# Kernel optimization log

Measured on AMD Instinct MI355X. Metric: run time of the kernel, lower is better.

Reference implementation:

```python
import jax, jax.numpy as jnp
import numpy as np

B, S, D, V, OOV = 32, 1024, 512, 50000, 1000
BN_EPS = 1e-5


def setup_inputs() -> dict:
    key = jax.random.key(0)
    ks = jax.random.split(key, 24)
    std = 0.02
    inp = {
        'dec_output': jax.random.normal(ks[0], (B, 1, D), jnp.float32),
        'dec_hid_h': jax.random.normal(ks[1], (1, B, D), jnp.float32),
        'dec_hid_c': jax.random.normal(ks[2], (1, B, D), jnp.float32),
        'dec_inp': jax.random.normal(ks[3], (B, 1, D), jnp.float32),
        'enc_op': jax.random.normal(ks[4], (B, S, 2 * D), jnp.float32),
        'enc_op1': jax.random.normal(ks[5], (B, S, 2 * D), jnp.float32),
        'src_inp': jax.random.randint(ks[6], (B, S), 0, V, jnp.int64) if jax.config.jax_enable_x64 else jax.random.randint(ks[6], (B, S), 0, V, jnp.int32),
        # mod_dec_op: Linear(2D -> 2D) with bias
        'W_dec': jax.random.normal(ks[7], (2 * D, 2 * D), jnp.float32) * std,
        'b_dec': jax.random.normal(ks[8], (2 * D,), jnp.float32) * std,
        # get_attn: Linear(2D -> 1), no bias
        'w_attn': jax.random.normal(ks[9], (2 * D,), jnp.float32) * std,
        # get_vocab: Linear(3D -> D) then Linear(D -> V-OOV)
        'W_v1': jax.random.normal(ks[10], (D, 3 * D), jnp.float32) * std,
        'b_v1': jax.random.normal(ks[11], (D,), jnp.float32) * std,
        'W_v2': jax.random.normal(ks[12], (V - OOV, D), jnp.float32) * std,
        'b_v2': jax.random.normal(ks[13], (V - OOV,), jnp.float32) * std,
        # p_gen: sigmoid(Linear([context(2D); dec_state(2D); dec_inp(D)] -> 1))
        'W_p': jax.random.normal(ks[14], (1, 5 * D), jnp.float32) * std,
        'b_p': jax.random.normal(ks[15], (1,), jnp.float32) * std,
        # BatchNorm1d(2D), eval mode
        'bn_gamma': jnp.ones((2 * D,), jnp.float32),
        'bn_beta': jnp.zeros((2 * D,), jnp.float32),
        'bn_mean': jax.random.normal(ks[16], (2 * D,), jnp.float32) * 0.1,
        'bn_var': jax.random.uniform(ks[17], (2 * D,), jnp.float32, 0.5, 1.5),
    }
    return inp


def reference(dec_output, dec_hid_h, dec_hid_c, dec_inp, enc_op, enc_op1, src_inp,
              W_dec, b_dec, w_attn, W_v1, b_v1, W_v2, b_v2, W_p, b_p,
              bn_gamma, bn_beta, bn_mean, bn_var):
    # dec_op: [B, 2D] = [h_b ; c_b]
    dec_op = jnp.concatenate([dec_hid_h[0], dec_hid_c[0]], axis=-1)
    dec_op1 = dec_op @ W_dec.T + b_dec                              # [B, 2D]
    features = jnp.tanh(enc_op1 + dec_op1[:, None, :])              # [B, S, 2D]
    attn = jax.nn.softmax(jnp.einsum('bsd,d->bs', features, w_attn), axis=-1)
    mask = (src_inp != 0).astype(attn.dtype)
    attn = attn * mask
    attn = attn / jnp.sum(attn, axis=1, keepdims=True)              # renormalize
    context = jnp.einsum('bs,bsd->bd', attn, enc_op)                # [B, 2D]
    context = (context - bn_mean) * jax.lax.rsqrt(bn_var + BN_EPS) * bn_gamma + bn_beta
    temp = jnp.concatenate([dec_output[:, 0, :], context], axis=-1)  # [B, 3D]
    logits = (temp @ W_v1.T + b_v1) @ W_v2.T + b_v2                 # [B, V-OOV]
    p_vocab = jax.nn.softmax(logits, axis=-1)
    p_vocab = jnp.concatenate([p_vocab, jnp.zeros((p_vocab.shape[0], OOV), p_vocab.dtype)], axis=-1)
    pg_in = jnp.concatenate([context, dec_op, dec_inp[:, 0, :]], axis=-1)  # [B, 5D]
    p_gen = jax.nn.sigmoid(pg_in @ W_p.T + b_p)                     # [B, 1]
    src_attn = (1.0 - p_gen) * attn                                  # [B, S]
    p_final = p_gen * p_vocab                                        # [B, V]
    rows = jnp.arange(p_final.shape[0])[:, None]
    p_final = p_final.at[rows, src_inp].add(src_attn)
    p_final = p_final + (p_final == 0).astype(p_final.dtype) * 1e-12
    return (p_final, attn, context)
```

## Files before the change

kernel.cpp:

```cpp
#include <hip/hip_runtime.h>

#define B    32
#define S    1024
#define D    512
#define D2   1024
#define D5   2560
#define V    50000
#define VO   49000
#define NCH  14
#define CHW  3500
#define NCHV 766

__device__ __forceinline__ float fast_tanh(float x){
    float e = __expf(2.0f * x);
    return 1.0f - __fdividef(2.0f, e + 1.0f);
}

__global__ __launch_bounds__(256) void gemm_nt(
    const float* __restrict__ W, int Nreal, int K,
    const float* __restrict__ xa, const float* __restrict__ xb,
    int xsplit, int xstra, int xstrb,
    float* __restrict__ parts, int KS)
{
    __shared__ float sW[16 * 260];
    __shared__ float sX[16 * 32];
    const int t    = threadIdx.x;
    const int lane = t & 63;
    const int v0   = blockIdx.x * 256;
    const int ks0  = blockIdx.y * KS;
    const int b0   = (t >> 6) * 8;

    const int vrow  = v0 + t;
    const size_t wb = (size_t)((vrow < Nreal) ? vrow : (Nreal - 1)) * K;

    float acc[4][8];
    #pragma unroll
    for (int i = 0; i < 4; ++i)
        #pragma unroll
        for (int j = 0; j < 8; ++j) acc[i][j] = 0.f;

    const int  xbi  = t >> 2;
    const int  xq   = t & 3;
    const bool xact = t < 128;

    float4 wreg[4];
    float  xreg[4];
    #pragma unroll
    for (int e = 0; e < 4; ++e) wreg[e] = *(const float4*)&W[wb + ks0 + e * 4];
    if (xact){
        #pragma unroll
        for (int e = 0; e < 4; ++e){
            int k = ks0 + xq * 4 + e;
            xreg[e] = (k < xsplit) ? xa[xbi * xstra + k] : xb[xbi * xstrb + (k - xsplit)];
        }
    }

    const int ntiles = KS >> 4;
    for (int tl = 0; tl < ntiles; ++tl){
        #pragma unroll
        for (int e = 0; e < 4; ++e){
            sW[(e * 4 + 0) * 260 + t] = wreg[e].x;
            sW[(e * 4 + 1) * 260 + t] = wreg[e].y;
            sW[(e * 4 + 2) * 260 + t] = wreg[e].z;
            sW[(e * 4 + 3) * 260 + t] = wreg[e].w;
        }
        if (xact){
            #pragma unroll
            for (int e = 0; e < 4; ++e) sX[(xq * 4 + e) * 32 + xbi] = xreg[e];
        }
        __syncthreads();
        if (tl + 1 < ntiles){
            int kn = ks0 + (tl + 1) * 16;
            #pragma unroll
            for (int e = 0; e < 4; ++e) wreg[e] = *(const float4*)&W[wb + kn + e * 4];
            if (xact){
                #pragma unroll
                for (int e = 0; e < 4; ++e){
                    int k = kn + xq * 4 + e;
                    xreg[e] = (k < xsplit) ? xa[xbi * xstra + k] : xb[xbi * xstrb + (k - xsplit)];
                }
            }
        }
        #pragma unroll
        for (int kk = 0; kk < 16; ++kk){
            const float4 w0 = *(const float4*)&sW[kk * 260 + lane * 4];
            const float4 x0 = *(const float4*)&sX[kk * 32 + b0];
            const float4 x1 = *(const float4*)&sX[kk * 32 + b0 + 4];
            const float wv[4] = {w0.x, w0.y, w0.z, w0.w};
            const float xv[8] = {x0.x, x0.y, x0.z, x0.w, x1.x, x1.y, x1.z, x1.w};
            #pragma unroll
            for (int i = 0; i < 4; ++i)
                #pragma unroll
                for (int j = 0; j < 8; ++j)
                    acc[i][j] += wv[i] * xv[j];
        }
        __syncthreads();
    }
    const int vbase = v0 + lane * 4;
    if (vbase < Nreal){
        const size_t pb = (size_t)blockIdx.y * B;
        #pragma unroll
        for (int j = 0; j < 8; ++j){
            float4 o = make_float4(acc[0][j], acc[1][j], acc[2][j], acc[3][j]);
            *(float4*)&parts[(pb + b0 + j) * (size_t)Nreal + vbase] = o;
        }
    }
}

__global__ void kreduce(const float* __restrict__ parts, float* __restrict__ out,
                        int n, int nsplit, const float* __restrict__ bias, int bmask){
    int i = blockIdx.x * 256 + threadIdx.x;
    if (i < n){
        float s = 0.f;
        for (int p = 0; p < nsplit; ++p) s += parts[(size_t)p * n + i];
        if (bias) s += bias[i & bmask];
        out[i] = s;
    }
}

__global__ void k2a_logit(const float* __restrict__ enc1, const float* __restrict__ dop1,
                          const float* __restrict__ bdec, const float* __restrict__ wat,
                          const int* __restrict__ src,
                          float* __restrict__ lg, float* __restrict__ pm,
                          float* __restrict__ ps){
    int b = blockIdx.x;
    int wave = threadIdx.x >> 6, lane = threadIdx.x & 63;
    int s0 = blockIdx.y * 16 + wave * 4;
    __shared__ float sd[D2], sw[D2];
    __shared__ float slog[16];
    for (int i = threadIdx.x; i < D2; i += 256){
        sd[i] = dop1[b * D2 + i] + bdec[i];
        sw[i] = wat[i];
    }
    __syncthreads();
    const float4* sd4 = (const float4*)sd;
    const float4* sw4 = (const float4*)sw;
    for (int r = 0; r < 4; ++r){
        int s = s0 + r;
        const float4* row = (const float4*)(enc1 + ((size_t)b * S + s) * D2);
        float acc = 0.f;
        #pragma unroll
        for (int i = 0; i < 4; ++i){
            int k4 = i * 64 + lane;
            float4 e = row[k4]; float4 dv = sd4[k4]; float4 wv = sw4[k4];
            acc += fast_tanh(e.x + dv.x) * wv.x + fast_tanh(e.y + dv.y) * wv.y
                 + fast_tanh(e.z + dv.z) * wv.z + fast_tanh(e.w + dv.w) * wv.w;
        }
        #pragma unroll
        for (int off = 32; off > 0; off >>= 1) acc += __shfl_down(acc, off, 64);
        if (lane == 0){
            lg[b * S + s] = acc;
            slog[wave * 4 + r] = acc;
        }
    }
    __syncthreads();
    if (threadIdx.x == 0){
        int sbase = blockIdx.y * 16;
        float m = -1e30f;
        #pragma unroll
        for (int i = 0; i < 16; ++i) m = fmaxf(m, slog[i]);
        float sum = 0.f;
        #pragma unroll
        for (int i = 0; i < 16; ++i){
            bool keep = src[b * S + sbase + i] != 0;
            sum += keep ? __expf(slog[i] - m) : 0.f;
        }
        pm[b * 64 + blockIdx.y] = m;
        ps[b * 64 + blockIdx.y] = sum;
    }
}

__global__ void k2c_attn_ctx(const float* __restrict__ enc, const float* __restrict__ lg,
                             const int* __restrict__ src, const float* __restrict__ pm,
                             const float* __restrict__ ps,
                             float* __restrict__ attn, float* __restrict__ part){
    int b = blockIdx.x, sp = blockIdx.y, t = threadIdx.x;
    __shared__ float sa[32];
    __shared__ float sMS[2];
    if (t < 64){
        float m = pm[b * 64 + t];
        float s = ps[b * 64 + t];
        float M = m;
        #pragma unroll
        for (int off = 1; off < 64; off <<= 1) M = fmaxf(M, __shfl_xor(M, off, 64));
        float sv = s * __expf(m - M);
        #pragma unroll
        for (int off = 1; off < 64; off <<= 1) sv += __shfl_xor(sv, off, 64);
        if (t == 0){ sMS[0] = M; sMS[1] = sv; }
    }
    __syncthreads();
    float M   = sMS[0];
    float inv = 1.0f / sMS[1];
    if (t < 32){
        int s = sp * 32 + t;
        float l = lg[b * S + s];
        bool keep = src[b * S + s] != 0;
        float a = keep ? __expf(l - M) * inv : 0.f;
        attn[b * S + s] = a;
        sa[t] = a;
    }
    __syncthreads();
    const float4* base = (const float4*)(enc + ((size_t)b * S + sp * 32) * D2);
    float4 acc = make_float4(0.f, 0.f, 0.f, 0.f);
    #pragma unroll 4
    for (int s = 0; s < 32; ++s){
        float a = sa[s];
        float4 e = base[s * (D2 / 4) + t];
        acc.x += a * e.x; acc.y += a * e.y; acc.z += a * e.z; acc.w += a * e.w;
    }
    ((float4*)(part + ((size_t)(b * 32 + sp)) * D2))[t] = acc;
}

__global__ void k2d_ctxbn(const float* __restrict__ part, const float* __restrict__ gamma,
                          const float* __restrict__ beta, const float* __restrict__ mean,
                          const float* __restrict__ var, float* __restrict__ ctx){
    int b = blockIdx.x, t = threadIdx.x;
    float4 acc = make_float4(0.f, 0.f, 0.f, 0.f);
    for (int sp = 0; sp < 32; ++sp){
        float4 p = ((const float4*)(part + ((size_t)(b * 32 + sp)) * D2))[t];
        acc.x += p.x; acc.y += p.y; acc.z += p.z; acc.w += p.w;
    }
    float4 g  = ((const float4*)gamma)[t];
    float4 be = ((const float4*)beta)[t];
    float4 mn = ((const float4*)mean)[t];
    float4 vr = ((const float4*)var)[t];
    acc.x = (acc.x - mn.x) * rsqrtf(vr.x + 1e-5f) * g.x + be.x;
    acc.y = (acc.y - mn.y) * rsqrtf(vr.y + 1e-5f) * g.y + be.y;
    acc.z = (acc.z - mn.z) * rsqrtf(vr.z + 1e-5f) * g.z + be.z;
    acc.w = (acc.w - mn.w) * rsqrtf(vr.w + 1e-5f) * g.w + be.w;
    ((float4*)(ctx + (size_t)b * D2))[t] = acc;
}

__global__ void k3r_pgen(const float* __restrict__ parts, float* __restrict__ out,
                         const float* __restrict__ bias,
                         const float* __restrict__ ctx, const float* __restrict__ h,
                         const float* __restrict__ c, const float* __restrict__ di,
                         const float* __restrict__ Wp, const float* __restrict__ bp,
                         float* __restrict__ pg){
    int t = threadIdx.x;
    if (blockIdx.x < 64){
        int i = blockIdx.x * 256 + t;
        float s = 0.f;
        for (int p = 0; p < 16; ++p) s += parts[(size_t)p * (B * D) + i];
        s += bias[i & (D - 1)];
        out[i] = s;
        return;
    }
    int b = blockIdx.x - 64;
    float acc = 0.f;
    for (int k = t; k < D5; k += 256){
        float x;
        if (k < D2)            x = ctx[b * D2 + k];
        else if (k < D2 + D)   x = h[b * D + (k - D2)];
        else if (k < 2 * D2)   x = c[b * D + (k - D2 - D)];
        else                   x = di[b * D + (k - 2 * D2)];
        acc += x * Wp[k];
    }
    __shared__ float red[256];
    red[t] = acc; __syncthreads();
    for (int o = 128; o > 0; o >>= 1){
        if (t < o) red[t] += red[t + o];
        __syncthreads();
    }
    if (t == 0){
        float z = red[0] + bp[0];
        pg[b] = 1.0f / (1.0f + __expf(-z));
    }
}

__global__ __launch_bounds__(128) void gemm_vocab64(
    const float* __restrict__ W, const float* __restrict__ hid,
    const float* __restrict__ b2, float* __restrict__ lred,
    float* __restrict__ mch, float* __restrict__ sch)
{
    __shared__ float sW[16 * 68];
    __shared__ float sX[16 * 32];
    const int t    = threadIdx.x;
    const int lane = t & 63;
    const int wave = t >> 6;
    const int v0   = blockIdx.x * 64;

    const int sr   = t & 63;
    const int sh   = (t >> 6) * 8;
    const int vrow = v0 + sr;
    const size_t wb = (size_t)((vrow < VO) ? vrow : (VO - 1)) * D + sh;

    const int xbi = t >> 2;
    const int xq  = (t & 3) * 4;

    float acc[16];
    #pragma unroll
    for (int j = 0; j < 16; ++j) acc[j] = 0.f;

    float4 wreg[2];
    float  xreg[4];
    wreg[0] = *(const float4*)&W[wb];
    wreg[1] = *(const float4*)&W[wb + 4];
    #pragma unroll
    for (int e = 0; e < 4; ++e) xreg[e] = hid[xbi * D + xq + e];

    for (int tl = 0; tl < 32; ++tl){
        sW[(sh + 0) * 68 + sr] = wreg[0].x;
        sW[(sh + 1) * 68 + sr] = wreg[0].y;
        sW[(sh + 2) * 68 + sr] = wreg[0].z;
        sW[(sh + 3) * 68 + sr] = wreg[0].w;
        sW[(sh + 4) * 68 + sr] = wreg[1].x;
        sW[(sh + 5) * 68 + sr] = wreg[1].y;
        sW[(sh + 6) * 68 + sr] = wreg[1].z;
        sW[(sh + 7) * 68 + sr] = wreg[1].w;
        #pragma unroll
        for (int e = 0; e < 4; ++e) sX[(xq + e) * 32 + xbi] = xreg[e];
        __syncthreads();
        if (tl + 1 < 32){
            const int kn = (tl + 1) * 16;
            wreg[0] = *(const float4*)&W[wb + kn];
            wreg[1] = *(const float4*)&W[wb + kn + 4];
            #pragma unroll
            for (int e = 0; e < 4; ++e) xreg[e] = hid[xbi * D + kn + xq + e];
        }
        #pragma unroll
        for (int kk = 0; kk < 16; ++kk){
            const float  w  = sW[kk * 68 + lane];
            const float4 x0 = *(const float4*)&sX[kk * 32 + wave * 16 + 0];
            const float4 x1 = *(const float4*)&sX[kk * 32 + wave * 16 + 4];
            const float4 x2 = *(const float4*)&sX[kk * 32 + wave * 16 + 8];
            const float4 x3 = *(const float4*)&sX[kk * 32 + wave * 16 + 12];
            acc[0]  += w * x0.x; acc[1]  += w * x0.y; acc[2]  += w * x0.z; acc[3]  += w * x0.w;
            acc[4]  += w * x1.x; acc[5]  += w * x1.y; acc[6]  += w * x1.z; acc[7]  += w * x1.w;
            acc[8]  += w * x2.x; acc[9]  += w * x2.y; acc[10] += w * x2.z; acc[11] += w * x2.w;
            acc[12] += w * x3.x; acc[13] += w * x3.y; acc[14] += w * x3.z; acc[15] += w * x3.w;
        }
        __syncthreads();
    }

    const int  va    = v0 + lane;
    const bool valid = va < VO;
    const float b2v  = valid ? b2[va] : 0.f;

    #pragma unroll
    for (int j = 0; j < 16; ++j){
        const int b = wave * 16 + j;
        float l = acc[j] + b2v;
        if (valid) lred[(size_t)b * VO + va] = l;
        float m = valid ? l : -1e30f;
        #pragma unroll
        for (int off = 1; off < 64; off <<= 1) m = fmaxf(m, __shfl_xor(m, off, 64));
        float sv = valid ? __expf(l - m) : 0.f;
        #pragma unroll
        for (int off = 1; off < 64; off <<= 1) sv += __shfl_xor(sv, off, 64);
        if (lane == 0){
            mch[b * NCHV + blockIdx.x] = m;
            sch[b * NCHV + blockIdx.x] = sv;
        }
    }
}

__global__ void kC_final2(const float* __restrict__ lred, const float* __restrict__ mch,
                          const float* __restrict__ sch, const float* __restrict__ pg,
                          float* __restrict__ pf){
    int b = blockIdx.x, c = blockIdx.y, t = threadIdx.x;
    if (c == NCH){
        for (int v = VO + t; v < V; v += 256) pf[(size_t)b * V + v] = 0.f;
        return;
    }
    __shared__ float sm[256], ss[256];
    float m = -1e30f, s = 0.f;
    for (int ch = t; ch < NCHV; ch += 256){
        float mc = mch[b * NCHV + ch], sc = sch[b * NCHV + ch];
        float M = fmaxf(m, mc);
        s = s * __expf(m - M) + sc * __expf(mc - M);
        m = M;
    }
    sm[t] = m; ss[t] = s; __syncthreads();
    for (int o = 128; o > 0; o >>= 1){
        if (t < o){
            float m1 = sm[t], m2 = sm[t + o];
            float M = fmaxf(m1, m2);
            ss[t] = ss[t] * __expf(m1 - M) + ss[t + o] * __expf(m2 - M);
            sm[t] = M;
        }
        __syncthreads();
    }
    float M  = sm[0];
    float sc = pg[b] / ss[0];
    for (int v = c * CHW + t; v < (c + 1) * CHW; v += 256)
        pf[(size_t)b * V + v] = sc * __expf(lred[(size_t)b * VO + v] - M);
}

__global__ void k5b_scatter(const int* __restrict__ src, const float* __restrict__ attn,
                            const float* __restrict__ pg, float* __restrict__ pf){
    int b = blockIdx.x, t = threadIdx.x;
    float c1 = 1.0f - pg[b];
    for (int s = t; s < S; s += 256){
        int idx = src[b * S + s];
        atomicAdd(&pf[(size_t)b * V + idx], c1 * attn[b * S + s]);
    }
}

extern "C" void kernel_launch(void* const* d_in, const int* in_sizes, int n_in,
                              void* d_out, int out_size, void* d_ws, size_t ws_size,
                              hipStream_t stream){
    (void)in_sizes; (void)n_in; (void)out_size; (void)ws_size;
    const float* dec_output = (const float*)d_in[0];
    const float* h          = (const float*)d_in[1];
    const float* c          = (const float*)d_in[2];
    const float* dec_inp    = (const float*)d_in[3];
    const float* enc_op     = (const float*)d_in[4];
    const float* enc_op1    = (const float*)d_in[5];
    const int*   src        = (const int*)d_in[6];
    const float* W_dec      = (const float*)d_in[7];
    const float* b_dec      = (const float*)d_in[8];
    const float* w_attn     = (const float*)d_in[9];
    const float* W_v1       = (const float*)d_in[10];
    const float* b_v1       = (const float*)d_in[11];
    const float* W_v2       = (const float*)d_in[12];
    const float* b_v2       = (const float*)d_in[13];
    const float* W_p        = (const float*)d_in[14];
    const float* b_p        = (const float*)d_in[15];
    const float* bn_g       = (const float*)d_in[16];
    const float* bn_b       = (const float*)d_in[17];
    const float* bn_m       = (const float*)d_in[18];
    const float* bn_v       = (const float*)d_in[19];

    float* ws = (float*)d_ws;
    float* p1       = ws;
    float* dec_op1  = ws + 524288;
    float* p3       = ws + 557056;
    float* hidden   = ws + 819200;
    float* lred     = ws + 835584;
    float* attn_lg  = ws + 2403584;
    float* ctx_part = ws + 2436352;
    float* pg       = ws + 3484928;
    float* mch      = ws + 3484960;
    float* sch      = ws + 3509472;
    float* pm       = ws + 3533984;
    float* ps       = ws + 3536032;

    float* pf   = (float*)d_out;
    float* attn = pf + 1600000;
    float* ctx  = pf + 1632768;

    gemm_nt <<<dim3(4, 16),  256, 0, stream>>>(W_dec, D2, D2, h, c, D, D, D, p1, 64);
    kreduce <<<128,          256, 0, stream>>>(p1, dec_op1, B * D2, 16, nullptr, 0);
    k2a_logit<<<dim3(B, 64), 256, 0, stream>>>(enc_op1, dec_op1, b_dec, w_attn, src,
                                               attn_lg, pm, ps);
    k2c_attn_ctx<<<dim3(B, 32), 256, 0, stream>>>(enc_op, attn_lg, src, pm, ps,
                                                  attn, ctx_part);
    k2d_ctxbn<<<B,           256, 0, stream>>>(ctx_part, bn_g, bn_b, bn_m, bn_v, ctx);
    gemm_nt <<<dim3(2, 16),  256, 0, stream>>>(W_v1, D, D + D2, dec_output, ctx,
                                               D, D, D2, p3, 96);
    k3r_pgen<<<96,           256, 0, stream>>>(p3, hidden, b_v1,
                                               ctx, h, c, dec_inp, W_p, b_p, pg);
    gemm_vocab64<<<NCHV,     128, 0, stream>>>(W_v2, hidden, b_v2, lred, mch, sch);
    kC_final2<<<dim3(B, NCH + 1), 256, 0, stream>>>(lred, mch, sch, pg, pf);
    k5b_scatter<<<B,         256, 0, stream>>>(src, attn, pg, pf);
}
```

Measured before the change: 506.8 us.

## Widen vocab GEMM tile to 192 rows with 256 threads and 256 blocks

The vocab projection kernel now has each 256-thread block cover 192 vocabulary rows instead of 64. That gives 256 blocks, about one per CU. Staging is split: 192 threads load W rows and 64 threads load the hidden activations. Each wave accumulates 3x8 outputs instead of 1x16, and the per-block softmax partials are merged with an online max/sum shuffle reduction. The goal is better W reuse per block and fewer partial chunks, at the cost of more registers per thread and less total parallelism.

Result: faster. 475.4 us (-6.2%).

```diff
diff --git a/kernel.cpp b/kernel.cpp
--- a/kernel.cpp
+++ b/kernel.cpp
@@ -9,7 +9,8 @@
 #define VO   49000
 #define NCH  14
 #define CHW  3500
-#define NCHV 766
+#define NCHV 256
+#define VT   192
 
 __device__ __forceinline__ float fast_tanh(float x){
     float e = __expf(2.0f * x);
@@ -268,89 +269,121 @@
     }
 }
 
-__global__ __launch_bounds__(128) void gemm_vocab64(
+__global__ __launch_bounds__(256) void gemm_vocab192(
     const float* __restrict__ W, const float* __restrict__ hid,
     const float* __restrict__ b2, float* __restrict__ lred,
     float* __restrict__ mch, float* __restrict__ sch)
 {
-    __shared__ float sW[16 * 68];
+    __shared__ float sW[16 * VT];
     __shared__ float sX[16 * 32];
     const int t    = threadIdx.x;
     const int lane = t & 63;
     const int wave = t >> 6;
-    const int v0   = blockIdx.x * 64;
-
-    const int sr   = t & 63;
-    const int sh   = (t >> 6) * 8;
-    const int vrow = v0 + sr;
-    const size_t wb = (size_t)((vrow < VO) ? vrow : (VO - 1)) * D + sh;
-
-    const int xbi = t >> 2;
-    const int xq  = (t & 3) * 4;
-
-    float acc[16];
+    const int v0   = blockIdx.x * VT;
+    const int b0   = wave * 8;
+
+    float acc[3][8];
     #pragma unroll
-    for (int j = 0; j < 16; ++j) acc[j] = 0.f;
-
-    float4 wreg[2];
-    float  xreg[4];
-    wreg[0] = *(const float4*)&W[wb];
-    wreg[1] = *(const float4*)&W[wb + 4];
-    #pragma unroll
-    for (int e = 0; e < 4; ++e) xreg[e] = hid[xbi * D + xq + e];
+    for (int i = 0; i < 3; ++i)
+        #pragma unroll
+        for (int j = 0; j < 8; ++j) acc[i][j] = 0.f;
+
+    const bool wstage = t < VT;
+    const int  wr     = t;
+    const int  vr     = v0 + wr;
+    const size_t wb   = (size_t)((vr < VO) ? vr : (VO - 1)) * D;
+    const int  u      = t - VT;
+    const int  xb     = u & 31;
+    const int  xk     = (u >> 5) * 8;
+
+    float4 wreg[4];
+    float  xreg[8];
+    if (wstage){
+        #pragma unroll
+        for (int e = 0; e < 4; ++e) wreg[e] = *(const float4*)&W[wb + e * 4];
+    } else {
+        #pragma unroll
+        for (int e = 0; e < 8; ++e) xreg[e] = hid[xb * D + xk + e];
+    }
 
     for (int tl = 0; tl < 32; ++tl){
-        sW[(sh + 0) * 68 + sr] = wreg[0].x;
-        sW[(sh + 1) * 68 + sr] = wreg[0].y;
-        sW[(sh + 2) * 68 + sr] = wreg[0].z;
-        sW[(sh + 3) * 68 + sr] = wreg[0].w;
-        sW[(sh + 4) * 68 + sr] = wreg[1].x;
-        sW[(sh + 5) * 68 + sr] = wreg[1].y;
-        sW[(sh + 6) * 68 + sr] = wreg[1].z;
-        sW[(sh + 7) * 68 + sr] = wreg[1].w;
-        #pragma unroll
-        for (int e = 0; e < 4; ++e) sX[(xq + e) * 32 + xbi] = xreg[e];
+        if (wstage){
+            #pragma unroll
+            for (int e = 0; e < 4; ++e){
+                sW[(e * 4 + 0) * VT + wr] = wreg[e].x;
+                sW[(e * 4 + 1) * VT + wr] = wreg[e].y;
+                sW[(e * 4 + 2) * VT + wr] = wreg[e].z;
+                sW[(e * 4 + 3) * VT + wr] = wreg[e].w;
+            }
+        } else {
+            #pragma unroll
+            for (int e = 0; e < 8; ++e) sX[(xk + e) * 32 + xb] = xreg[e];
+        }
         __syncthreads();
         if (tl + 1 < 32){
             const int kn = (tl + 1) * 16;
-            wreg[0] = *(const float4*)&W[wb + kn];
-            wreg[1] = *(const float4*)&W[wb + kn + 4];
-            #pragma unroll
-            for (int e = 0; e < 4; ++e) xreg[e] = hid[xbi * D + kn + xq + e];
+            if (wstage){
+                #pragma unroll
+                for (int e = 0; e < 4; ++e) wreg[e] = *(const float4*)&W[wb + kn + e * 4];
+            } else {
+                #pragma unroll
+                for (int e = 0; e < 8; ++e) xreg[e] = hid[xb * D + kn + xk + e];
+            }
         }
         #pragma unroll
         for (int kk = 0; kk < 16; ++kk){
-            const float  w  = sW[kk * 68 + lane];
-            const float4 x0 = *(const float4*)&sX[kk * 32 + wave * 16 + 0];
-            const float4 x1 = *(const float4*)&sX[kk * 32 + wave * 16 + 4];
-            const float4 x2 = *(const float4*)&sX[kk * 32 + wave * 16 + 8];
-            const float4 x3 = *(const float4*)&sX[kk * 32 + wave * 16 + 12];
-            acc[0]  += w * x0.x; acc[1]  += w * x0.y; acc[2]  += w * x0.z; acc[3]  += w * x0.w;
-            acc[4]  += w * x1.x; acc[5]  += w * x1.y; acc[6]  += w * x1.z; acc[7]  += w * x1.w;
-            acc[8]  += w * x2.x; acc[9]  += w * x2.y; acc[10] += w * x2.z; acc[11] += w * x2.w;
-            acc[12] += w * x3.x; acc[13] += w * x3.y; acc[14] += w * x3.z; acc[15] += w * x3.w;
-        }
-        __syncthreads();
-    }
-
-    const int  va    = v0 + lane;
-    const bool valid = va < VO;
-    const float b2v  = valid ? b2[va] : 0.f;
-
+            const float w0 = sW[kk * VT + lane];
+            const float w1 = sW[kk * VT + 64 + lane];
+            const float w2 = sW[kk * VT + 128 + lane];
+            const float4 x0 = *(const float4*)&sX[kk * 32 + b0];
+            const float4 x1 = *(const float4*)&sX[kk * 32 + b0 + 4];
+            const float xv[8] = {x0.x, x0.y, x0.z, x0.w, x1.x, x1.y, x1.z, x1.w};
+            #pragma unroll
+            for (int j = 0; j < 8; ++j){
+                acc[0][j] += w0 * xv[j];
+                acc[1][j] += w1 * xv[j];
+                acc[2][j] += w2 * xv[j];
+            }
+        }
+        __syncthreads();
+    }
+
+    bool  valid[3];
+    float bias[3];
     #pragma unroll
-    for (int j = 0; j < 16; ++j){
-        const int b = wave * 16 + j;
-        float l = acc[j] + b2v;
-        if (valid) lred[(size_t)b * VO + va] = l;
-        float m = valid ? l : -1e30f;
-        #pragma unroll
-        for (int off = 1; off < 64; off <<= 1) m = fmaxf(m, __shfl_xor(m, off, 64));
-        float sv = valid ? __expf(l - m) : 0.f;
-        #pragma unroll
-        for (int off = 1; off < 64; off <<= 1) sv += __shfl_xor(sv, off, 64);
+    for (int i = 0; i < 3; ++i){
+        int v = v0 + i * 64 + lane;
+        valid[i] = v < VO;
+        bias[i]  = valid[i] ? b2[v] : 0.f;
+    }
+    #pragma unroll
+    for (int j = 0; j < 8; ++j){
+        const int b = b0 + j;
+        float l[3];
+        float m = -1e30f;
+        #pragma unroll
+        for (int i = 0; i < 3; ++i){
+            l[i] = acc[i][j] + bias[i];
+            if (valid[i]){
+                lred[(size_t)b * VO + v0 + i * 64 + lane] = l[i];
+                m = fmaxf(m, l[i]);
+            }
+        }
+        float s = 0.f;
+        #pragma unroll
+        for (int i = 0; i < 3; ++i)
+            s += valid[i] ? __expf(l[i] - m) : 0.f;
+        #pragma unroll
+        for (int off = 1; off < 64; off <<= 1){
+            float m2 = __shfl_xor(m, off, 64);
+            float s2 = __shfl_xor(s, off, 64);
+            float M  = fmaxf(m, m2);
+            s = s * __expf(m - M) + s2 * __expf(m2 - M);
+            m = M;
+        }
         if (lane == 0){
             mch[b * NCHV + blockIdx.x] = m;
-            sch[b * NCHV + blockIdx.x] = sv;
+            sch[b * NCHV + blockIdx.x] = s;
         }
     }
 }
@@ -432,9 +465,9 @@
     float* ctx_part = ws + 2436352;
     float* pg       = ws + 3484928;
     float* mch      = ws + 3484960;
-    float* sch      = ws + 3509472;
-    float* pm       = ws + 3533984;
-    float* ps       = ws + 3536032;
+    float* sch      = ws + 3493152;
+    float* pm       = ws + 3501344;
+    float* ps       = ws + 3503392;
 
     float* pf   = (float*)d_out;
     float* attn = pf + 1600000;
@@ -451,7 +484,7 @@
                                                D, D, D2, p3, 96);
     k3r_pgen<<<96,           256, 0, stream>>>(p3, hidden, b_v1,
                                                ctx, h, c, dec_inp, W_p, b_p, pg);
-    gemm_vocab64<<<NCHV,     128, 0, stream>>>(W_v2, hidden, b_v2, lred, mch, sch);
+    gemm_vocab192<<<NCHV,    256, 0, stream>>>(W_v2, hidden, b_v2, lred, mch, sch);
     kC_final2<<<dim3(B, NCH + 1), 256, 0, stream>>>(lred, mch, sch, pg, pf);
     k5b_scatter<<<B,         256, 0, stream>>>(src, attn, pg, pf);
 }
```
